# Kernel optimization log

Measured on AMD Instinct MI355X. Metric: run time of the kernel, lower is better.

Reference implementation:

```python
import jax, jax.numpy as jnp
import numpy as np

EPS = 1e-20

def _log(t):
    return jnp.log(jnp.clip(t, EPS, None))

def setup_inputs() -> dict:
    key = jax.random.key(0)
    k1, k2 = jax.random.split(key)
    L, B, D = 1, 8192, 128
    a = jax.random.normal(k1, (L, B, D), dtype=jnp.float32)
    t = jax.random.normal(k2, (L, B, D), dtype=jnp.float32)
    # latents are L2-normalized (standard practice before this contrastive loss;
    # keeps exp(temp * sim) finite with init_temp=10)
    a = a / jnp.linalg.norm(a, axis=-1, keepdims=True)
    t = t / jnp.linalg.norm(t, axis=-1, keepdims=True)
    temperatures = jnp.full((1, 1, 1), np.log(10.0), dtype=jnp.float32)
    return {"audio_latents": a, "text_latents": t, "temperatures": temperatures}

def reference(audio_latents, text_latents, temperatures):
    # audio_latents, text_latents: (L, B, D); single-process so all_gather is identity
    L, B, D = audio_latents.shape
    N = L * B
    a = audio_latents.reshape(N, D)
    t = text_latents.reshape(N, D)
    # sims: (N, N); layers=1 so temperatures.exp() is a scalar broadcast
    sims = jnp.einsum('id,jd->ij', a, t) * jnp.exp(temperatures[0, 0, 0])
    exp_sims = jnp.exp(sims)
    numerator = jnp.diagonal(exp_sims)  # (N,)
    # decoupled contrastive learning: zero the diagonal before the denominators
    idx = jnp.arange(N)
    exp_masked = exp_sims.at[idx, idx].set(0.0)
    den_i = jnp.sum(exp_masked, axis=1)  # row sums (N,)
    den_j = jnp.sum(exp_masked, axis=0)  # col sums (N,)
    loss = -_log(numerator) + 0.5 * (_log(den_i) + _log(den_j))
    return jnp.mean(loss).reshape(1)  # matches reduce('1 n -> 1', 'mean')
```

## Files before the change

### kernel.cpp

```cpp
#include <hip/hip_runtime.h>
#include <hip/hip_bf16.h>


typedef __attribute__((ext_vector_type(8))) int   v8i;
typedef __attribute__((ext_vector_type(4))) int   v4i;
typedef __attribute__((ext_vector_type(4))) float f32x4;

#define SCALE_ONE 0x7F7F7F7F

#define GLD16(g, l) __builtin_amdgcn_global_load_lds(                         \
    (const __attribute__((address_space(1))) unsigned int*)(const void*)(g),  \
    (__attribute__((address_space(3))) unsigned int*)(void*)(l), 16, 0, 0)

__device__ __forceinline__ float fast_exp2(float x) {
#if __has_builtin(__builtin_amdgcn_exp2f)
    return __builtin_amdgcn_exp2f(x);
#else
    return __expf(x * 0.69314718056f);
#endif
}

template <int CTRL>
__device__ __forceinline__ float dpp_sr_add(float v) {
    int s = __builtin_amdgcn_update_dpp(0, __float_as_int(v), CTRL, 0xf, 0xf, true);
    return v + __int_as_float(s);
}
__device__ __forceinline__ float row16_sum(float v) {
    v = dpp_sr_add<0x111>(v);
    v = dpp_sr_add<0x112>(v);
    v = dpp_sr_add<0x114>(v);
    v = dpp_sr_add<0x118>(v);
    return v;
}

__global__ void convert_pack(const float* __restrict__ a,
                             const float* __restrict__ t,
                             const float* __restrict__ temps,
                             unsigned char* __restrict__ oa,
                             unsigned char* __restrict__ ot) {
    int idx = blockIdx.x * 256 + threadIdx.x;
    const bool isT = (idx >> 16) != 0;
    const float* src = isT ? t : a;
    unsigned char* dst = isT ? ot : oa;
    const float s = isT ? 1.0f : (__expf(temps[0]) * 1.44269504f);
    int loc = idx & 65535;
    int tile = loc >> 7, sub = loc & 127;
    int lane = sub >> 1, h = sub & 1;
    int row = tile * 16 + (lane & 15);
    int k0  = (lane >> 4) * 32 + h * 16;
    const float4* s4 = reinterpret_cast<const float4*>(src + row * 128 + k0);
    unsigned w[4];
#pragma unroll
    for (int q = 0; q < 4; ++q) {
        float4 f = s4[q];
        int v = __builtin_amdgcn_cvt_pk_fp8_f32(f.x * s, f.y * s, 0, false);
        v = __builtin_amdgcn_cvt_pk_fp8_f32(f.z * s, f.w * s, v, true);
        w[q] = (unsigned)v;
    }
    int off = isT ? (tile * 2048 + h * 1024 + lane * 16)
                  : (tile * 2048 + lane * 32 + h * 16);
    *reinterpret_cast<uint4*>(dst + off) = make_uint4(w[0], w[1], w[2], w[3]);
}

__device__ __forceinline__ v8i ld_tile(const unsigned char* lds, int tile, int lane) {
    v4i lo = *reinterpret_cast<const v4i*>(lds + tile * 2048 + lane * 16);
    v4i hi = *reinterpret_cast<const v4i*>(lds + tile * 2048 + 1024 + lane * 16);
    v8i r;
    r[0] = lo[0]; r[1] = lo[1]; r[2] = lo[2]; r[3] = lo[3];
    r[4] = hi[0]; r[5] = hi[1]; r[6] = hi[2]; r[7] = hi[3];
    return r;
}

#define LD2(BUF, T0)                                                     \
    BUF[0] = ld_tile(ldsT, (T0), lane);                                  \
    BUF[1] = ld_tile(ldsT, (T0) + 1, lane);

#define PHASE(BF, COLBASE)                                               \
  {                                                                      \
    f32x4 acc[4][2];                                                     \
    _Pragma("unroll") for (int m = 0; m < 4; ++m)                        \
      _Pragma("unroll") for (int n = 0; n < 2; ++n)                      \
        acc[m][n] = (f32x4){0.f, 0.f, 0.f, 0.f};                         \
    _Pragma("unroll") for (int m = 0; m < 4; ++m)                        \
      _Pragma("unroll") for (int n = 0; n < 2; ++n)                      \
        acc[m][n] = __builtin_amdgcn_mfma_scale_f32_16x16x128_f8f6f4(    \
            af[m], BF[n], acc[m][n], 0, 0, 0, SCALE_ONE, 0, SCALE_ONE);  \
    float csum[2] = {0.f, 0.f};                                          \
    _Pragma("unroll") for (int m = 0; m < 4; ++m)                        \
      _Pragma("unroll") for (int n = 0; n < 2; ++n)                      \
        _Pragma("unroll") for (int jj = 0; jj < 4; ++jj) {               \
          float v = fast_exp2(acc[m][n][jj]);                            \
          rsum[m][jj] += v;                                              \
          csum[n] += v;                                                  \
        }                                                                \
    _Pragma("unroll") for (int n = 0; n < 2; ++n) {                      \
      float v = csum[n];                                                 \
      v += __shfl_xor(v, 16); v += __shfl_xor(v, 32);                    \
      if (lane < 16) {                                                   \
        int col = (COLBASE + n) * 16 + lcol;                             \
        Pj[col * 128 + rs] = v;                                          \
      }                                                                  \
    }                                                                    \
  }

__global__ void __launch_bounds__(256)
gemm_exp(const unsigned char* __restrict__ Ap, const unsigned char* __restrict__ Tp,
         float* __restrict__ Pi, float* __restrict__ Pj) {
    __shared__ unsigned char ldsT[32768];
    const int tid = threadIdx.x;
    const int wave = tid >> 6, lane = tid & 63;
    const int krow = lane >> 4, lcol = lane & 15;
    const int fid = blockIdx.x;
    const int vid = (fid & 7) * 128 + (fid >> 3);
    const int j  = vid >> 5;
    const int rg = vid & 31;
    const int rs = rg * 4 + wave;

    const unsigned char* gT = Tp + j * 16 * 2048;
#pragma unroll
    for (int tt = 0; tt < 4; ++tt) {
        int tile = wave * 4 + tt;
        GLD16(gT + tile * 2048 + lane * 16,        &ldsT[tile * 2048]);
        GLD16(gT + tile * 2048 + 1024 + lane * 16, &ldsT[tile * 2048 + 1024]);
    }

    v8i af[4];
#pragma unroll
    for (int m = 0; m < 4; ++m)
        af[m] = *reinterpret_cast<const v8i*>(Ap + (rs * 4 + m) * 2048 + lane * 32);

    __syncthreads();

    float rsum[4][4] = {};
    v8i bfA[2], bfB[2];

    LD2(bfA, 0)
    LD2(bfB, 2)
    PHASE(bfA, j * 16 + 0)
    LD2(bfA, 4)
    PHASE(bfB, j * 16 + 2)
    LD2(bfB, 6)
    PHASE(bfA, j * 16 + 4)
    LD2(bfA, 8)
    PHASE(bfB, j * 16 + 6)
    LD2(bfB, 10)
    PHASE(bfA, j * 16 + 8)
    LD2(bfA, 12)
    PHASE(bfB, j * 16 + 10)
    LD2(bfB, 14)
    PHASE(bfA, j * 16 + 12)
    PHASE(bfB, j * 16 + 14)

#pragma unroll
    for (int m = 0; m < 4; ++m)
#pragma unroll
        for (int jj = 0; jj < 4; ++jj) {
            float v = row16_sum(rsum[m][jj]);
            if (lcol == 15) {
                int row = rs * 64 + m * 16 + krow * 4 + jj;
                Pi[row * 32 + j] = v;
            }
        }
}

__global__ void finalize_rows(const float* __restrict__ a, const float* __restrict__ t,
                              const float* __restrict__ temps,
                              const float* __restrict__ Pi, const float* __restrict__ Pj,
                              float* __restrict__ loss) {
    const int r = blockIdx.x * 4 + (threadIdx.x >> 6);
    const int l = threadIdx.x & 63;
    const float sc = __expf(temps[0]);
    float deni = (l < 32) ? Pi[r * 32 + l] : 0.f;
    float denj = Pj[r * 128 + l] + Pj[r * 128 + 64 + l];
    float dotp = a[r * 128 + l] * t[r * 128 + l]
               + a[r * 128 + 64 + l] * t[r * 128 + 64 + l];
#pragma unroll
    for (int m = 1; m < 64; m <<= 1) {
        deni += __shfl_xor(deni, m);
        denj += __shfl_xor(denj, m);
        dotp += __shfl_xor(dotp, m);
    }
    if (l == 0) {
        float diag = __expf(sc * dotp);
        float di = fmaxf(deni - diag, 1e-20f);
        float dj = fmaxf(denj - diag, 1e-20f);
        loss[r] = -sc * dotp + 0.5f * (__logf(di) + __logf(dj));
    }
}

__global__ void reduce_loss(const float* __restrict__ loss, float* __restrict__ out) {
    __shared__ float wsum[16];
    const int tid = threadIdx.x;
    float s = 0.f;
#pragma unroll
    for (int i = 0; i < 8; ++i) s += loss[tid + i * 1024];
#pragma unroll
    for (int m = 1; m < 64; m <<= 1) s += __shfl_xor(s, m);
    if ((tid & 63) == 0) wsum[tid >> 6] = s;
    __syncthreads();
    if (tid == 0) {
        float acc = 0.f;
#pragma unroll
        for (int w = 0; w < 16; ++w) acc += wsum[w];
        out[0] = acc * (1.0f / 8192.0f);
    }
}

extern "C" void kernel_launch(void* const* d_in, const int* in_sizes, int n_in,
                              void* d_out, int out_size, void* d_ws, size_t ws_size,
                              hipStream_t stream) {
    const float* a     = (const float*)d_in[0];
    const float* t     = (const float*)d_in[1];
    const float* temps = (const float*)d_in[2];
    float* out = (float*)d_out;

    char* ws = (char*)d_ws;
    unsigned char* Ap = (unsigned char*)(ws);
    unsigned char* Tp = (unsigned char*)(ws + (1u << 20));
    float* Pi  = (float*)(ws + (2u << 20));
    float* Pj  = (float*)(ws + (4u << 20));
    float* los = (float*)(ws + (8u << 20));

    convert_pack<<<512, 256, 0, stream>>>(a, t, temps, Ap, Tp);
    gemm_exp<<<1024, 256, 0, stream>>>(Ap, Tp, Pi, Pj);
    finalize_rows<<<2048, 256, 0, stream>>>(a, t, temps, Pi, Pj, los);
    reduce_loss<<<1, 1024, 0, stream>>>(los, out);
}
```

Before: 42.14 us.

## Load B tiles directly from global, transpose Pj layout, fuse loss reduction

```diff
diff --git a/kernel.cpp b/kernel.cpp
--- a/kernel.cpp
+++ b/kernel.cpp
@@ -3,14 +3,9 @@
 
 
 typedef __attribute__((ext_vector_type(8))) int   v8i;
-typedef __attribute__((ext_vector_type(4))) int   v4i;
 typedef __attribute__((ext_vector_type(4))) float f32x4;
 
 #define SCALE_ONE 0x7F7F7F7F
-
-#define GLD16(g, l) __builtin_amdgcn_global_load_lds(                         \
-    (const __attribute__((address_space(1))) unsigned int*)(const void*)(g),  \
-    (__attribute__((address_space(3))) unsigned int*)(void*)(l), 16, 0, 0)
 
 __device__ __forceinline__ float fast_exp2(float x) {
 #if __has_builtin(__builtin_amdgcn_exp2f)
@@ -57,25 +52,15 @@
         v = __builtin_amdgcn_cvt_pk_fp8_f32(f.z * s, f.w * s, v, true);
         w[q] = (unsigned)v;
     }
-    int off = isT ? (tile * 2048 + h * 1024 + lane * 16)
-                  : (tile * 2048 + lane * 32 + h * 16);
-    *reinterpret_cast<uint4*>(dst + off) = make_uint4(w[0], w[1], w[2], w[3]);
-}
-
-__device__ __forceinline__ v8i ld_tile(const unsigned char* lds, int tile, int lane) {
-    v4i lo = *reinterpret_cast<const v4i*>(lds + tile * 2048 + lane * 16);
-    v4i hi = *reinterpret_cast<const v4i*>(lds + tile * 2048 + 1024 + lane * 16);
-    v8i r;
-    r[0] = lo[0]; r[1] = lo[1]; r[2] = lo[2]; r[3] = lo[3];
-    r[4] = hi[0]; r[5] = hi[1]; r[6] = hi[2]; r[7] = hi[3];
-    return r;
+    *reinterpret_cast<uint4*>(dst + tile * 2048 + lane * 32 + h * 16) =
+        make_uint4(w[0], w[1], w[2], w[3]);
 }
 
 #define LD2(BUF, T0)                                                     \
-    BUF[0] = ld_tile(ldsT, (T0), lane);                                  \
-    BUF[1] = ld_tile(ldsT, (T0) + 1, lane);
-
-#define PHASE(BF, COLBASE)                                               \
+    BUF[0] = *reinterpret_cast<const v8i*>(tb + (T0) * 2048);            \
+    BUF[1] = *reinterpret_cast<const v8i*>(tb + (T0 + 1) * 2048);
+
+#define PH(BF, CS)                                                       \
   {                                                                      \
     f32x4 acc[4][2];                                                     \
     _Pragma("unroll") for (int m = 0; m < 4; ++m)                        \
@@ -85,28 +70,34 @@
       _Pragma("unroll") for (int n = 0; n < 2; ++n)                      \
         acc[m][n] = __builtin_amdgcn_mfma_scale_f32_16x16x128_f8f6f4(    \
             af[m], BF[n], acc[m][n], 0, 0, 0, SCALE_ONE, 0, SCALE_ONE);  \
-    float csum[2] = {0.f, 0.f};                                          \
+    CS[0] = 0.f; CS[1] = 0.f;                                            \
     _Pragma("unroll") for (int m = 0; m < 4; ++m)                        \
       _Pragma("unroll") for (int n = 0; n < 2; ++n)                      \
         _Pragma("unroll") for (int jj = 0; jj < 4; ++jj) {               \
           float v = fast_exp2(acc[m][n][jj]);                            \
           rsum[m][jj] += v;                                              \
-          csum[n] += v;                                                  \
+          CS[n] += v;                                                    \
         }                                                                \
-    _Pragma("unroll") for (int n = 0; n < 2; ++n) {                      \
-      float v = csum[n];                                                 \
-      v += __shfl_xor(v, 16); v += __shfl_xor(v, 32);                    \
-      if (lane < 16) {                                                   \
-        int col = (COLBASE + n) * 16 + lcol;                             \
-        Pj[col * 128 + rs] = v;                                          \
-      }                                                                  \
+  }
+
+#define TAIL4(BASE)                                                      \
+  {                                                                      \
+    float t0 = csA[0], t1 = csA[1], t2 = csB[0], t3 = csB[1];            \
+    t0 += __shfl_xor(t0, 16); t1 += __shfl_xor(t1, 16);                  \
+    t2 += __shfl_xor(t2, 16); t3 += __shfl_xor(t3, 16);                  \
+    t0 += __shfl_xor(t0, 32); t1 += __shfl_xor(t1, 32);                  \
+    t2 += __shfl_xor(t2, 32); t3 += __shfl_xor(t3, 32);                  \
+    if (lane < 16) {                                                     \
+      pjb[((BASE) + 0) * 16 + lcol] = t0;                                \
+      pjb[((BASE) + 1) * 16 + lcol] = t1;                                \
+      pjb[((BASE) + 2) * 16 + lcol] = t2;                                \
+      pjb[((BASE) + 3) * 16 + lcol] = t3;                                \
     }                                                                    \
   }
 
 __global__ void __launch_bounds__(256)
 gemm_exp(const unsigned char* __restrict__ Ap, const unsigned char* __restrict__ Tp,
          float* __restrict__ Pi, float* __restrict__ Pj) {
-    __shared__ unsigned char ldsT[32768];
     const int tid = threadIdx.x;
     const int wave = tid >> 6, lane = tid & 63;
     const int krow = lane >> 4, lcol = lane & 15;
@@ -116,40 +107,38 @@
     const int rg = vid & 31;
     const int rs = rg * 4 + wave;
 
-    const unsigned char* gT = Tp + j * 16 * 2048;
-#pragma unroll
-    for (int tt = 0; tt < 4; ++tt) {
-        int tile = wave * 4 + tt;
-        GLD16(gT + tile * 2048 + lane * 16,        &ldsT[tile * 2048]);
-        GLD16(gT + tile * 2048 + 1024 + lane * 16, &ldsT[tile * 2048 + 1024]);
-    }
-
     v8i af[4];
 #pragma unroll
     for (int m = 0; m < 4; ++m)
         af[m] = *reinterpret_cast<const v8i*>(Ap + (rs * 4 + m) * 2048 + lane * 32);
 
-    __syncthreads();
+    const unsigned char* tb = Tp + j * 16 * 2048 + lane * 32;
+    float* pjb = Pj + rs * 8192 + j * 256;
 
     float rsum[4][4] = {};
+    float csA[2], csB[2];
     v8i bfA[2], bfB[2];
 
     LD2(bfA, 0)
     LD2(bfB, 2)
-    PHASE(bfA, j * 16 + 0)
+    PH(bfA, csA)
     LD2(bfA, 4)
-    PHASE(bfB, j * 16 + 2)
+    PH(bfB, csB)
+    TAIL4(0)
     LD2(bfB, 6)
-    PHASE(bfA, j * 16 + 4)
+    PH(bfA, csA)
     LD2(bfA, 8)
-    PHASE(bfB, j * 16 + 6)
+    PH(bfB, csB)
+    TAIL4(4)
     LD2(bfB, 10)
-    PHASE(bfA, j * 16 + 8)
+    PH(bfA, csA)
     LD2(bfA, 12)
-    PHASE(bfB, j * 16 + 10)
+    PH(bfB, csB)
+    TAIL4(8)
     LD2(bfB, 14)
-    PHASE(bfA, j * 16 + 12)
-    PHASE(bfB, j * 16 + 14)
+    PH(bfA, csA)
+    PH(bfB, csB)
+    TAIL4(12)
 
 #pragma unroll
     for (int m = 0; m < 4; ++m)
@@ -166,44 +155,61 @@
 __global__ void finalize_rows(const float* __restrict__ a, const float* __restrict__ t,
                               const float* __restrict__ temps,
                               const float* __restrict__ Pi, const float* __restrict__ Pj,
-                              float* __restrict__ loss) {
-    const int r = blockIdx.x * 4 + (threadIdx.x >> 6);
-    const int l = threadIdx.x & 63;
+                              float* __restrict__ blockLoss) {
+    __shared__ float ldsJ[4][64];
+    __shared__ float wsum[4];
+    const int tid = threadIdx.x;
+    const int r0 = blockIdx.x * 64;
     const float sc = __expf(temps[0]);
-    float deni = (l < 32) ? Pi[r * 32 + l] : 0.f;
-    float denj = Pj[r * 128 + l] + Pj[r * 128 + 64 + l];
-    float dotp = a[r * 128 + l] * t[r * 128 + l]
-               + a[r * 128 + 64 + l] * t[r * 128 + 64 + l];
-#pragma unroll
-    for (int m = 1; m < 64; m <<= 1) {
-        deni += __shfl_xor(deni, m);
-        denj += __shfl_xor(denj, m);
-        dotp += __shfl_xor(dotp, m);
-    }
-    if (l == 0) {
+
+    {
+        const int c = tid & 63, g = tid >> 6;
+        float dj = 0.f;
+#pragma unroll 4
+        for (int rr = 0; rr < 32; ++rr)
+            dj += Pj[(g * 32 + rr) * 8192 + r0 + c];
+        ldsJ[g][c] = dj;
+    }
+    __syncthreads();
+
+    const int row = r0 + (tid >> 2), q = tid & 3;
+    const float4* pi4 = reinterpret_cast<const float4*>(Pi + row * 32 + q * 8);
+    float4 p0 = pi4[0], p1 = pi4[1];
+    float deni = (p0.x + p0.y + p0.z + p0.w) + (p1.x + p1.y + p1.z + p1.w);
+    float dotp = 0.f;
+    const float4* a4 = reinterpret_cast<const float4*>(a + row * 128 + q * 32);
+    const float4* t4 = reinterpret_cast<const float4*>(t + row * 128 + q * 32);
+#pragma unroll
+    for (int u = 0; u < 8; ++u) {
+        float4 av = a4[u], tv = t4[u];
+        dotp += av.x * tv.x + av.y * tv.y + av.z * tv.z + av.w * tv.w;
+    }
+    deni += __shfl_xor(deni, 1); deni += __shfl_xor(deni, 2);
+    dotp += __shfl_xor(dotp, 1); dotp += __shfl_xor(dotp, 2);
+
+    float loss = 0.f;
+    if (q == 0) {
+        float denj = (ldsJ[0][row - r0] + ldsJ[1][row - r0])
+                   + (ldsJ[2][row - r0] + ldsJ[3][row - r0]);
         float diag = __expf(sc * dotp);
         float di = fmaxf(deni - diag, 1e-20f);
         float dj = fmaxf(denj - diag, 1e-20f);
-        loss[r] = -sc * dotp + 0.5f * (__logf(di) + __logf(dj));
-    }
-}
-
-__global__ void reduce_loss(const float* __restrict__ loss, float* __restrict__ out) {
-    __shared__ float wsum[16];
+        loss = -sc * dotp + 0.5f * (__logf(di) + __logf(dj));
+    }
+#pragma unroll
+    for (int m = 1; m < 64; m <<= 1) loss += __shfl_xor(loss, m);
+    if ((tid & 63) == 0) wsum[tid >> 6] = loss;
+    __syncthreads();
+    if (tid == 0)
+        blockLoss[blockIdx.x] = (wsum[0] + wsum[1]) + (wsum[2] + wsum[3]);
+}
+
+__global__ void reduce_loss(const float* __restrict__ blockLoss, float* __restrict__ out) {
     const int tid = threadIdx.x;
-    float s = 0.f;
-#pragma unroll
-    for (int i = 0; i < 8; ++i) s += loss[tid + i * 1024];
+    float s = blockLoss[tid] + blockLoss[tid + 64];
 #pragma unroll
     for (int m = 1; m < 64; m <<= 1) s += __shfl_xor(s, m);
-    if ((tid & 63) == 0) wsum[tid >> 6] = s;
-    __syncthreads();
-    if (tid == 0) {
-        float acc = 0.f;
-#pragma unroll
-        for (int w = 0; w < 16; ++w) acc += wsum[w];
-        out[0] = acc * (1.0f / 8192.0f);
-    }
+    if (tid == 0) out[0] = s * (1.0f / 8192.0f);
 }
 
 extern "C" void kernel_launch(void* const* d_in, const int* in_sizes, int n_in,
@@ -219,10 +225,10 @@
     unsigned char* Tp = (unsigned char*)(ws + (1u << 20));
     float* Pi  = (float*)(ws + (2u << 20));
     float* Pj  = (float*)(ws + (4u << 20));
-    float* los = (float*)(ws + (8u << 20));
+    float* bl  = (float*)(ws + (8u << 20));
 
     convert_pack<<<512, 256, 0, stream>>>(a, t, temps, Ap, Tp);
     gemm_exp<<<1024, 256, 0, stream>>>(Ap, Tp, Pi, Pj);
-    finalize_rows<<<2048, 256, 0, stream>>>(a, t, temps, Pi, Pj, los);
-    reduce_loss<<<1, 1024, 0, stream>>>(los, out);
-}
+    finalize_rows<<<128, 256, 0, stream>>>(a, t, temps, Pi, Pj, bl);
+    reduce_loss<<<1, 64, 0, stream>>>(bl, out);
+}
```

After: 42.41 us. Within noise of the previous version (+0.6%).
